# Kernel optimization log

Measured on AMD Instinct MI355X. Metric: run time of the kernel, lower is better.

The kernel has to match this reference:

```python
import jax, jax.numpy as jnp
import numpy as np

B_, C_, H_, W_ = 8, 128, 64, 64
OUT_ = 128
D_MODEL = C_ // 4        # 32, per-chunk channels fed to Mamba
D_STATE = 16
D_CONV = 4
D_INNER = 2 * D_MODEL    # expand=2 -> 64
DT_RANK = max(1, -(-D_MODEL // 16))  # ceil(32/16)=2
SE_RED = 2


def _ln(x, g, b):
    m = x.mean(-1, keepdims=True)
    v = jnp.var(x, axis=-1, keepdims=True)
    return (x - m) / jnp.sqrt(v + 1e-5) * g + b


def _mamba(u, in_W, conv_W, conv_b, xproj_W, dt_W, dt_b, A_log, D_p, out_W):
    # u: (B, L, d_model)
    Bsz, L, _ = u.shape
    xz = u @ in_W.T                                   # (B,L,2*d_inner)
    x, z = jnp.split(xz, 2, axis=-1)
    # causal depthwise conv1d along L
    xc = jnp.swapaxes(x, 1, 2)                        # (B,d_inner,L)
    xc = jax.lax.conv_general_dilated(
        xc, conv_W, (1,), [(D_CONV - 1, 0)],
        feature_group_count=D_INNER,
        dimension_numbers=('NCH', 'OIH', 'NCH'))
    x = jax.nn.silu(jnp.swapaxes(xc + conv_b[None, :, None], 1, 2))
    x_dbl = x @ xproj_W.T                             # (B,L,dt_rank+2*d_state)
    dt, Bm, Cm = jnp.split(x_dbl, [DT_RANK, DT_RANK + D_STATE], axis=-1)
    dt = jax.nn.softplus(dt @ dt_W.T + dt_b)          # (B,L,d_inner)
    A = -jnp.exp(A_log)                               # (d_inner,d_state)
    dA = jnp.exp(dt[..., None] * A)                   # (B,L,d_inner,d_state)
    dBu = dt[..., None] * Bm[:, :, None, :] * x[..., None]

    def step(h, inp):
        dA_t, dBu_t, C_t = inp
        h = dA_t * h + dBu_t                          # (B,d_inner,d_state)
        return h, jnp.einsum('bds,bs->bd', h, C_t)

    h0 = jnp.zeros((Bsz, D_INNER, D_STATE), dtype=x.dtype)
    _, ys = jax.lax.scan(step, h0, (jnp.swapaxes(dA, 0, 1), jnp.swapaxes(dBu, 0, 1), jnp.swapaxes(Cm, 0, 1)))
    y = jnp.swapaxes(ys, 0, 1) + x * D_p
    y = y * jax.nn.silu(z)
    return y @ out_W.T


def _branch(xi, skip_scale, se_W1, se_W2, mp):
    M1 = _mamba(xi, *mp)                              # (B,L,c)
    M2 = skip_scale * xi
    # SE: adaptive avg-pool over spatial == mean over tokens; cat over channels
    y = jnp.concatenate([M1, M2], axis=-1).mean(axis=1)   # (B,2c)
    y = jax.nn.sigmoid(jax.nn.relu(y @ se_W1.T) @ se_W2.T)
    g1, g2 = jnp.split(y, 2, axis=-1)
    return g1[:, None, :] * M1 + g2[:, None, :] * M2


def _pvm(x, norm_g, norm_b, proj_W, proj_b, skip_scale, se_W1, se_W2,
         in_W, conv_W, conv_b, xproj_W, dt_W, dt_b, A_log, D_p, out_W):
    B, C, H, W = x.shape
    L = H * W
    xf = jnp.swapaxes(x.reshape(B, C, L), 1, 2)       # (B,L,C)
    xn = _ln(xf, norm_g, norm_b)
    mp = (in_W, conv_W, conv_b, xproj_W, dt_W, dt_b, A_log, D_p, out_W)
    outs = [_branch(c, skip_scale, se_W1, se_W2, mp) for c in jnp.split(xn, 4, axis=2)]
    xm = jnp.concatenate(outs, axis=2)                # (B,L,C)
    xm = _ln(xm, norm_g, norm_b)
    xm = xm @ proj_W.T + proj_b                       # (B,L,out)
    return jnp.swapaxes(xm, 1, 2).reshape(B, proj_W.shape[0], H, W)


def setup_inputs():
    key = jax.random.key(0)
    ks = jax.random.split(key, 10)
    p = {}
    p['x'] = jax.random.normal(ks[0], (B_, C_, H_, W_), jnp.float32)
    p['norm_g'] = jnp.ones((C_,), jnp.float32)
    p['norm_b'] = jnp.zeros((C_,), jnp.float32)
    p['proj_W'] = jax.random.normal(ks[1], (OUT_, C_), jnp.float32) * 0.05
    p['proj_b'] = jnp.zeros((OUT_,), jnp.float32)
    p['skip_scale'] = jnp.ones((1,), jnp.float32)
    p['se_W1'] = jax.random.normal(ks[2], (SE_RED, 2 * D_MODEL), jnp.float32) * 0.1
    p['se_W2'] = jax.random.normal(ks[3], (2 * D_MODEL, SE_RED), jnp.float32) * 0.1
    p['in_W'] = jax.random.normal(ks[4], (2 * D_INNER, D_MODEL), jnp.float32) * 0.1
    p['conv_W'] = jax.random.normal(ks[5], (D_INNER, 1, D_CONV), jnp.float32) * 0.2
    p['conv_b'] = jnp.zeros((D_INNER,), jnp.float32)
    p['xproj_W'] = jax.random.normal(ks[6], (DT_RANK + 2 * D_STATE, D_INNER), jnp.float32) * 0.1
    p['dt_W'] = jax.random.normal(ks[7], (D_INNER, DT_RANK), jnp.float32) * 0.1
    p['dt_b'] = jnp.full((D_INNER,), -4.6, jnp.float32)  # softplus(-4.6) ~ 0.01 init dt
    p['A_log'] = jnp.log(jnp.broadcast_to(jnp.arange(1.0, D_STATE + 1.0, dtype=jnp.float32), (D_INNER, D_STATE)))
    p['D_p'] = jnp.ones((D_INNER,), jnp.float32)
    p['out_W'] = jax.random.normal(ks[8], (D_MODEL, D_INNER), jnp.float32) * 0.1
    return p


def reference(x, norm_g, norm_b, proj_W, proj_b, skip_scale, se_W1, se_W2,
              in_W, conv_W, conv_b, xproj_W, dt_W, dt_b, A_log, D_p, out_W):
    return _pvm(x, norm_g, norm_b, proj_W, proj_b, skip_scale, se_W1, se_W2,
                in_W, conv_W, conv_b, xproj_W, dt_W, dt_b, A_log, D_p, out_W)
```

## Files before the change

### kernel.cpp

```cpp
#include <hip/hip_runtime.h>
#include <math.h>

typedef _Float16 h16;

#define DEV static __device__ __forceinline__

constexpr int B_ = 8, C_ = 128, L_ = 4096, OUT_ = 128;
constexpr int NCH = 4, DM = 32, DS = 16, DI = 64;
constexpr int NI = 32;
constexpr int NSEG = 128;
constexpr int SL = L_ / NSEG;

DEV float sigmoidf_(float x) { return 1.f / (1.f + __expf(-x)); }
DEV float siluf_(float x) { return x * sigmoidf_(x); }
DEV float softplusf_(float x) { return (x > 20.f) ? x : __logf(1.f + __expf(x)); }

template <int CTRL>
DEV float dpp_add_(float x) {
  int v = __builtin_amdgcn_update_dpp(0, __float_as_int(x), CTRL, 0xf, 0xf, false);
  return x + __int_as_float(v);
}

typedef __attribute__((ext_vector_type(8))) _Float16 f16x8;
typedef __attribute__((ext_vector_type(4))) _Float16 f16x4;
typedef __attribute__((ext_vector_type(4))) float f32x4;

DEV void powladder_(float E, float* out) {
  float E2 = E * E;
  float E4 = E2 * E2;
  float E8 = E4 * E4;
  float E3 = E2 * E;
  out[0] = E;       out[1] = E2;      out[2] = E3;      out[3] = E4;
  out[4] = E4 * E;  out[5] = E4 * E2; out[6] = E4 * E3; out[7] = E8;
  out[8] = E8 * E;  out[9] = E8 * E2; out[10] = E8 * E3; out[11] = E8 * E4;
  out[12] = E8 * out[4]; out[13] = E8 * out[5]; out[14] = E8 * out[6];
  out[15] = E8 * E8;
}

DEV void powladder8_(float E, float* out) {
  float E2 = E * E, E3 = E2 * E, E4 = E2 * E2;
  out[0] = E; out[1] = E2; out[2] = E3; out[3] = E4;
  out[4] = E4 * E; out[5] = E4 * E2; out[6] = E4 * E3; out[7] = E4 * E4;
}

__global__ __launch_bounds__(256) void k1_ln(
    const float* __restrict__ x, const float* __restrict__ gn,
    const float* __restrict__ bn, const float* __restrict__ in_W,
    const float* __restrict__ xproj_W, const float* __restrict__ out_W,
    const float* __restrict__ proj_W, const float* __restrict__ A_log,
    h16* __restrict__ WH, float* __restrict__ AVT, h16* __restrict__ XNH,
    float* __restrict__ SUMXN) {
  int bid = blockIdx.x;
  int tid = threadIdx.x;
  if (bid >= B_ * 64) {
    int g = (bid - B_ * 64) * 256 + tid;
    if (g < 1024) AVT[g] = -__expf(A_log[g]);
    if (g < 4096) {
      WH[g] = (h16)in_W[g];
    } else if (g < 7168) {
      int j = g - 4096;
      int r = j >> 6;
      WH[g] = (r < 34) ? (h16)xproj_W[r * 64 + (j & 63)] : (h16)0.f;
    } else if (g < 9216) {
      WH[g] = (h16)out_W[g - 7168];
    } else if (g < 25600) {
      WH[g] = (h16)proj_W[g - 9216];
    }
    return;
  }
  int b = bid >> 6, tile = bid & 63;
  int t0 = tile * 64;
  __shared__ float xT[128][65];
  __shared__ float gnS[128], bnS[128];
  __shared__ float red[256];
  if (tid < 128) { gnS[tid] = gn[tid]; bnS[tid] = bn[tid]; }
  for (int k = tid; k < 8192; k += 256) {
    int c = k >> 6, tt = k & 63;
    xT[c][tt] = x[((size_t)(b * C_ + c)) * L_ + t0 + tt];
  }
  __syncthreads();
  {
    int tok = tid >> 2, q = tid & 3;
    float s = 0.f, qq = 0.f;
#pragma unroll
    for (int j = 0; j < 32; ++j) {
      float v = xT[q + 4 * j][tok];
      s += v; qq += v * v;
    }
    s = dpp_add_<0xB1>(s); qq = dpp_add_<0xB1>(qq);
    s = dpp_add_<0x4E>(s); qq = dpp_add_<0x4E>(qq);
    float m = s * (1.f / 128.f);
    float var = qq * (1.f / 128.f) - m * m;
    float rs = rsqrtf(var + 1e-5f);
#pragma unroll
    for (int j = 0; j < 32; ++j) {
      int c = q + 4 * j;
      float v = xT[c][tok];
      xT[c][tok] = (v - m) * rs * gnS[c] + bnS[c];
    }
  }
  __syncthreads();
  float acc = 0.f;
  int cfix = tid & 127;
  for (int k = tid; k < 8192; k += 256) {
    int tt = k >> 7, c = k & 127;
    acc += xT[c][tt];
  }
  for (int k = tid; k < 1024; k += 256) {
    int tt = k >> 4, c8 = (k & 15) * 8;
    f16x8 hv;
#pragma unroll
    for (int j = 0; j < 8; ++j) hv[j] = (_Float16)xT[c8 + j][tt];
    *(f16x8*)&XNH[((size_t)(b * L_ + t0 + tt)) * C_ + c8] = hv;
  }
  red[tid] = acc;
  __syncthreads();
  if (tid < 128) atomicAdd(&SUMXN[b * C_ + cfix], red[tid] + red[tid + 128]);
}

__global__ __launch_bounds__(256) void k2_prep(
    const h16* __restrict__ WH, const float* __restrict__ conv_W,
    const float* __restrict__ conv_b, const float* __restrict__ dt_W,
    const float* __restrict__ dt_b, const float* __restrict__ AVT,
    const h16* __restrict__ XNH, h16* __restrict__ SX2, h16* __restrict__ SDT2,
    h16* __restrict__ SB2, h16* __restrict__ SC2, h16* __restrict__ SZ2,
    h16* __restrict__ Pp, h16* __restrict__ Qp) {
  int bid = blockIdx.x;
  int i = bid >> 6, tile = bid & 63;
  int b = i >> 2, ch = i & 3;
  int t0 = tile * 64;
  int tid = threadIdx.x;
  int w = __builtin_amdgcn_readfirstlane(tid >> 6);
  int lane = tid & 63;

  __shared__ __attribute__((aligned(16))) union {
    _Float16 uH[80][40];
    float xdS[64][36];
    _Float16 zL[64][72];
  } U;
  __shared__ __attribute__((aligned(16))) _Float16 preH[68][68];
  __shared__ __attribute__((aligned(16))) _Float16 xH[64][72];
  __shared__ float convWS[64][4];
  __shared__ float dtWS[64][2];
  __shared__ float dtbS[64], cbS[64];

  convWS[tid >> 2][tid & 3] = conv_W[tid];
  if (tid < 128) dtWS[tid >> 1][tid & 1] = dt_W[tid];
  if (tid < 64) { dtbS[tid] = dt_b[tid]; cbS[tid] = conv_b[tid]; }
  const h16* xnh = XNH + (size_t)b * L_ * C_ + ch * DM;
  for (int k = tid; k < 320; k += 256) {
    int r = k >> 2, c8 = (k & 3) * 8;
    int tg = t0 - 3 + r;
    f16x8 v = {0, 0, 0, 0, 0, 0, 0, 0};
    if (r < 67 && tg >= 0) v = *(const f16x8*)&xnh[(size_t)tg * C_ + c8];
    *(f16x8*)&U.uH[r][c8] = v;
  }
  __syncthreads();

  int rsel = lane & 15, ksel = (lane >> 4) * 8;
  {
    int nt = w;
    f16x8 bf = *(const f16x8*)&WH[(size_t)(nt * 16 + rsel) * 32 + ksel];
    int row0q = (lane >> 4) << 2;
    int col = nt * 16 + rsel;
#pragma unroll
    for (int mt = 0; mt < 5; ++mt) {
      f16x8 af = *(const f16x8*)&U.uH[mt * 16 + rsel][ksel];
      f32x4 acc = {0.f, 0.f, 0.f, 0.f};
      acc = __builtin_amdgcn_mfma_f32_16x16x32_f16(af, bf, acc, 0, 0, 0);
      int row0 = mt * 16 + row0q;
#pragma unroll
      for (int r = 0; r < 4; ++r) {
        int row = row0 + r;
        if (row < 67) preH[row][col] = (_Float16)acc[r];
      }
    }
  }
  f32x4 zacc[4];
  {
    f16x8 bf = *(const f16x8*)&U.uH[3 + w * 16 + rsel][ksel];
#pragma unroll
    for (int mt = 0; mt < 4; ++mt) {
      f16x8 af = *(const f16x8*)&WH[(size_t)(64 + mt * 16 + rsel) * 32 + ksel];
      f32x4 acc = {0.f, 0.f, 0.f, 0.f};
      zacc[mt] = __builtin_amdgcn_mfma_f32_16x16x32_f16(af, bf, acc, 0, 0, 0);
    }
  }
  __syncthreads();

  h16* SXp = SX2 + ((size_t)i * L_ + t0) * DI;
  for (int k = tid; k < 4096; k += 256) {
    int r = k >> 6, d = k & 63;
    float v = cbS[d];
#pragma unroll
    for (int j = 0; j < 4; ++j) v = fmaf(convWS[d][j], (float)preH[r + j][d], v);
    v = siluf_(v);
    xH[r][d] = (_Float16)v;
    SXp[(size_t)r * DI + d] = (h16)v;
  }
  __syncthreads();

  {
    int mt = w;
    f16x8 a0 = *(const f16x8*)&xH[mt * 16 + rsel][ksel];
    f16x8 a1 = *(const f16x8*)&xH[mt * 16 + rsel][32 + ksel];
    int row0 = mt * 16 + ((lane >> 4) << 2);
#pragma unroll
    for (int nt = 0; nt < 3; ++nt) {
      const h16* wp = WH + 4096 + (size_t)(nt * 16 + rsel) * 64;
      f16x8 b0 = *(const f16x8*)&wp[ksel];
      f16x8 b1 = *(const f16x8*)&wp[32 + ksel];
      f32x4 acc = {0.f, 0.f, 0.f, 0.f};
      acc = __builtin_amdgcn_mfma_f32_16x16x32_f16(a0, b0, acc, 0, 0, 0);
      acc = __builtin_amdgcn_mfma_f32_16x16x32_f16(a1, b1, acc, 0, 0, 0);
      int col = nt * 16 + rsel;
      if (col < 34) {
#pragma unroll
        for (int r = 0; r < 4; ++r) U.xdS[row0 + r][col] = acc[r];
      }
    }
  }
  __syncthreads();

  h16* dtL = (h16*)&preH[0][0];
  h16* SDTp = SDT2 + ((size_t)i * L_ + t0) * DI;
  for (int k = tid; k < 4096; k += 256) {
    int d = k & 63, r = k >> 6;
    float raw = fmaf(U.xdS[r][0], dtWS[d][0], fmaf(U.xdS[r][1], dtWS[d][1], dtbS[d]));
    float dtv = softplusf_(raw);
    dtL[r * 68 + d] = (_Float16)dtv;
    SDTp[(size_t)r * DI + d] = (h16)dtv;
  }
  h16* SBp = SB2 + ((size_t)i * L_ + t0) * DS;
  h16* SCp = SC2 + ((size_t)i * L_ + t0) * DS;
  for (int k = tid; k < 1024; k += 256) {
    int s = k & 15, r = k >> 4;
    SBp[(size_t)r * DS + s] = (h16)U.xdS[r][2 + s];
    SCp[(size_t)r * DS + s] = (h16)U.xdS[r][18 + s];
  }
  __syncthreads();

  {
    int seg = w >> 1, shalf = w & 1;
    int s0 = shalf * 8;
    float Av[16];
    {
      const float* avp = AVT + lane * 16;
#pragma unroll
      for (int j = 0; j < 4; ++j) *(float4*)&Av[4 * j] = *(const float4*)(avp + 4 * j);
    }
    float A0 = Av[0];
    bool okf = true;
#pragma unroll
    for (int s = 0; s < 16; ++s)
      okf &= fabsf(Av[s] - (float)(s + 1) * A0) <= 1e-4f * fabsf(Av[s]);
    int fastp = __all(okf ? 1 : 0);
    float h[8];
#pragma unroll
    for (int j = 0; j < 8; ++j) h[j] = 0.f;
    float sdt = 0.f;
    int rowbase = seg * SL;
    for (int t = 0; t < SL; ++t) {
      int row = rowbase + t;
      float dt = (float)dtL[row * 68 + lane];
      float xv = (float)xH[row][lane];
      float dtx = dt * xv;
      float dA[8];
      if (fastp) {
        powladder8_(__expf(A0 * dt), dA);
        if (shalf) {
          float E8 = dA[7];
#pragma unroll
          for (int j = 0; j < 8; ++j) dA[j] *= E8;
        }
      } else {
#pragma unroll
        for (int j = 0; j < 8; ++j) dA[j] = __expf(Av[s0 + j] * dt);
      }
      const float* brow = &U.xdS[row][2 + s0];
#pragma unroll
      for (int j = 0; j < 8; ++j) h[j] = fmaf(dA[j], h[j], dtx * brow[j]);
      sdt += dt;
    }
    float P[8];
    if (fastp) {
      powladder8_(__expf(A0 * sdt), P);
      if (shalf) {
        float E8 = P[7];
#pragma unroll
        for (int j = 0; j < 8; ++j) P[j] *= E8;
      }
    } else {
#pragma unroll
      for (int j = 0; j < 8; ++j) P[j] = __expf(Av[s0 + j] * sdt);
    }
    int segg = tile * 2 + seg;
    size_t base = (((size_t)i * NSEG + segg) * DI + lane) * DS + s0;
    f16x8 ph, qh;
#pragma unroll
    for (int j = 0; j < 8; ++j) { ph[j] = (_Float16)P[j]; qh[j] = (_Float16)h[j]; }
    *(f16x8*)(Pp + base) = ph;
    *(f16x8*)(Qp + base) = qh;
  }
  __syncthreads();

  {
    int tok = w * 16 + rsel;
    int zq = (lane >> 4) << 2;
#pragma unroll
    for (int mt = 0; mt < 4; ++mt) {
      f16x4 pk;
#pragma unroll
      for (int r = 0; r < 4; ++r) pk[r] = (_Float16)siluf_(zacc[mt][r]);
      *(f16x4*)&U.zL[tok][mt * 16 + zq] = pk;
    }
  }
  __syncthreads();
  h16* SZp = SZ2 + ((size_t)i * L_ + t0) * DI;
  for (int k = tid; k < 512; k += 256) {
    int r = k >> 3, dblk = (k & 7) * 8;
    f16x8 v = *(const f16x8*)&U.zL[r][dblk];
    *(f16x8*)&SZp[(size_t)r * DI + dblk] = v;
  }
}

__global__ __launch_bounds__(64) void k3b_comb(h16* __restrict__ Pp,
                                               const h16* __restrict__ Qp) {
  int g = blockIdx.x * 64 + threadIdx.x;
  int ds = g & 1023;
  int i = g >> 10;
  size_t base = (size_t)i * NSEG * DI * DS + ds;
  constexpr int SST = DI * DS;
  float H = 0.f;
  for (int sb = 0; sb < NSEG; sb += 16) {
    float Pv[16], Qv[16];
#pragma unroll
    for (int j = 0; j < 16; ++j) {
      size_t a = base + (size_t)(sb + j) * SST;
      Pv[j] = (float)Pp[a];
      Qv[j] = (float)Qp[a];
    }
#pragma unroll
    for (int j = 0; j < 16; ++j) {
      size_t a = base + (size_t)(sb + j) * SST;
      Pp[a] = (h16)H;
      H = fmaf(Pv[j], H, Qv[j]);
    }
  }
}

__global__ __launch_bounds__(256) void k3c_scan(
    const float* __restrict__ AVT, const h16* __restrict__ SDT2,
    const h16* __restrict__ SX2, const h16* __restrict__ SB2,
    const h16* __restrict__ SC2, const h16* __restrict__ SZ2,
    const float* __restrict__ D_p, const h16* __restrict__ H0p,
    h16* __restrict__ YS2, float* __restrict__ SUMYF) {
  int bid = blockIdx.x;
  int i = bid >> 5, sg = bid & 31;
  int tid = threadIdx.x;
  int w = tid >> 6, lane = tid & 63;
  int seg = sg * 4 + w;
  int t0 = seg * SL;
  __shared__ float rowS[4][SL][36];
  {
    int tk = lane & 31, hf = lane >> 5;
    const h16* p = (hf ? SC2 : SB2) + ((size_t)i * L_ + t0 + tk) * DS;
    float4 r0 = *(const float4*)p;
    float4 r1 = *(const float4*)(p + 8);
    const h16* hp0 = (const h16*)&r0;
    const h16* hp1 = (const h16*)&r1;
#pragma unroll
    for (int s = 0; s < 8; ++s) {
      rowS[w][tk][hf * 16 + s] = (float)hp0[s];
      rowS[w][tk][hf * 16 + 8 + s] = (float)hp1[s];
    }
  }
  __syncthreads();
  float Av[16];
  {
    const float* avp = AVT + lane * 16;
#pragma unroll
    for (int j = 0; j < 4; ++j) *(float4*)&Av[4 * j] = *(const float4*)(avp + 4 * j);
  }
  float A0 = Av[0];
  bool okf = true;
#pragma unroll
  for (int s = 0; s < 16; ++s) okf &= fabsf(Av[s] - (float)(s + 1) * A0) <= 1e-4f * fabsf(Av[s]);
  int fastp = __all(okf ? 1 : 0);
  float Dp = D_p[lane];
  float h[16];
  {
    const h16* hp = H0p + (((size_t)i * NSEG + seg) * DI + lane) * DS;
    f16x8 h0a = *(const f16x8*)hp;
    f16x8 h0b = *(const f16x8*)(hp + 8);
#pragma unroll
    for (int j = 0; j < 8; ++j) { h[j] = (float)h0a[j]; h[8 + j] = (float)h0b[j]; }
  }
  const h16* pdt = SDT2 + ((size_t)i * L_ + t0) * DI + lane;
  const h16* pxx = SX2 + ((size_t)i * L_ + t0) * DI + lane;
  const h16* pzz = SZ2 + ((size_t)i * L_ + t0) * DI + lane;
  h16* pys = YS2 + ((size_t)i * L_ + t0) * DI + lane;
  float dtc = (float)pdt[0], xvc = (float)pxx[0], zvc = (float)pzz[0];
  float sum = 0.f;
  for (int t = 0; t < SL; ++t) {
    float dt = dtc, xv = xvc, zv = zvc;
    if (t < SL - 1) {
      dtc = (float)pdt[(t + 1) * DI];
      xvc = (float)pxx[(t + 1) * DI];
      zvc = (float)pzz[(t + 1) * DI];
    }
    const float* row = &rowS[w][t][0];
    float Bv[16], Cv[16];
#pragma unroll
    for (int j = 0; j < 4; ++j) {
      *(float4*)&Bv[4 * j] = *(const float4*)(row + 4 * j);
      *(float4*)&Cv[4 * j] = *(const float4*)(row + 16 + 4 * j);
    }
    float dtx = dt * xv;
    float dA[16];
    if (fastp) {
      powladder_(__expf(A0 * dt), dA);
    } else {
#pragma unroll
      for (int s = 0; s < 16; ++s) dA[s] = __expf(Av[s] * dt);
    }
    float y0 = 0.f, y1 = 0.f, y2 = 0.f, y3 = 0.f;
#pragma unroll
    for (int s = 0; s < 16; s += 4) {
      h[s] = fmaf(dA[s], h[s], dtx * Bv[s]);       y0 = fmaf(h[s], Cv[s], y0);
      h[s + 1] = fmaf(dA[s + 1], h[s + 1], dtx * Bv[s + 1]); y1 = fmaf(h[s + 1], Cv[s + 1], y1);
      h[s + 2] = fmaf(dA[s + 2], h[s + 2], dtx * Bv[s + 2]); y2 = fmaf(h[s + 2], Cv[s + 2], y2);
      h[s + 3] = fmaf(dA[s + 3], h[s + 3], dtx * Bv[s + 3]); y3 = fmaf(h[s + 3], Cv[s + 3], y3);
    }
    float y = (y0 + y1) + (y2 + y3);
    float yf = fmaf(xv, Dp, y) * zv;
    pys[(size_t)t * DI] = (h16)yf;
    sum += yf;
  }
  atomicAdd(&SUMYF[i * DI + lane], sum);
}

__global__ __launch_bounds__(256) void k56_comb_proj(
    const float* __restrict__ out_W, const float* __restrict__ skip_p,
    const float* __restrict__ se_W1, const float* __restrict__ se_W2,
    const float* __restrict__ SUMYF, const float* __restrict__ SUMXN,
    const h16* __restrict__ YS2, const float* __restrict__ gn,
    const float* __restrict__ bn, const h16* __restrict__ WH,
    const float* __restrict__ proj_b, const h16* __restrict__ XNH,
    float* __restrict__ out) {
  int bid = blockIdx.x;
  int b = bid >> 6, tile = bid & 63;
  int t0 = tile * 64;
  int tid = threadIdx.x;
  int w = __builtin_amdgcn_readfirstlane(tid >> 6);
  int lane = tid & 63;
  __shared__ __attribute__((aligned(16))) union {
    float xmS[64][132];
    _Float16 projH[64][136];
  } U;
  __shared__ __attribute__((aligned(16))) union {
    struct {
      _Float16 yH[64][72];
      _Float16 owH[32][72];
    } pre;
    _Float16 xmH[64][136];
  } V;
  __shared__ float gAll[4][64];
  __shared__ float gnS[128], bnS[128];
  float* catS = (float*)&V.pre.yH[0][0];
  float* seL = catS + 256;

  if (tid < 128) { gnS[tid] = gn[tid]; bnS[tid] = bn[tid]; }
  for (int k = tid; k < 256; k += 256) {
    int r = k >> 3, c8 = (k & 7) * 8;
    *(f16x8*)&V.pre.owH[r][c8] = *(const f16x8*)&WH[7168 + r * 64 + c8];
  }
  const h16* xmh = XNH + (size_t)b * L_ * C_;
  for (int k = tid; k < 1024; k += 256) {
    int tt = k >> 4, c8 = (k & 15) * 8;
    f16x8 hv = *(const f16x8*)&xmh[(size_t)(t0 + tt) * C_ + c8];
#pragma unroll
    for (int j = 0; j < 8; ++j) U.xmS[tt][c8 + j] = (float)hv[j];
  }
  {
    int ch = tid >> 6, j = tid & 63;
    float invL = 1.f / (float)L_;
    if (j < 32) {
      const float* sy = SUMYF + (b * 4 + ch) * DI;
      const float* ow = out_W + j * 64;
      float acc = 0.f;
#pragma unroll
      for (int dd = 0; dd < 64; ++dd) acc = fmaf(sy[dd], ow[dd], acc);
      catS[ch * 64 + j] = acc * invL;
    } else {
      catS[ch * 64 + j] = skip_p[0] * SUMXN[b * C_ + ch * DM + (j - 32)] * invL;
    }
  }
  __syncthreads();
  if (tid < 8) {
    int ch = tid >> 1, r = tid & 1;
    float acc = 0.f;
#pragma unroll
    for (int k = 0; k < 64; ++k) acc = fmaf(catS[ch * 64 + k], se_W1[r * 64 + k], acc);
    seL[tid] = fmaxf(acc, 0.f);
  }
  __syncthreads();
  {
    int ch = tid >> 6, j = tid & 63;
    gAll[ch][j] = sigmoidf_(fmaf(seL[ch * 2], se_W2[j * 2], seL[ch * 2 + 1] * se_W2[j * 2 + 1]));
  }
  __syncthreads();

  int rsel = lane & 15, ksel = (lane >> 4) * 8;
  float skip = skip_p[0];
  for (int ch = 0; ch < 4; ++ch) {
    const h16* py = YS2 + ((size_t)(b * 4 + ch) * L_ + t0) * DI;
    for (int k = tid; k < 512; k += 256) {
      int tt = k >> 3, dblk = (k & 7) * 8;
      *(f16x8*)&V.pre.yH[tt][dblk] = *(const f16x8*)&py[(size_t)tt * DI + dblk];
    }
    __syncthreads();
    f16x8 a0 = *(const f16x8*)&V.pre.yH[w * 16 + rsel][ksel];
    f16x8 a1 = *(const f16x8*)&V.pre.yH[w * 16 + rsel][32 + ksel];
    int row0 = w * 16 + ((lane >> 4) << 2);
#pragma unroll
    for (int nt = 0; nt < 2; ++nt) {
      f16x8 b0 = *(const f16x8*)&V.pre.owH[nt * 16 + rsel][ksel];
      f16x8 b1 = *(const f16x8*)&V.pre.owH[nt * 16 + rsel][32 + ksel];
      f32x4 acc = {0.f, 0.f, 0.f, 0.f};
      acc = __builtin_amdgcn_mfma_f32_16x16x32_f16(a0, b0, acc, 0, 0, 0);
      acc = __builtin_amdgcn_mfma_f32_16x16x32_f16(a1, b1, acc, 0, 0, 0);
      int o = nt * 16 + rsel;
      float g1 = gAll[ch][o], g2s = gAll[ch][32 + o] * skip;
      int cc = ch * 32 + o;
#pragma unroll
      for (int r = 0; r < 4; ++r) {
        int tok = row0 + r;
        U.xmS[tok][cc] = g1 * acc[r] + g2s * U.xmS[tok][cc];
      }
    }
    __syncthreads();
  }

  {
    int tok = tid >> 2, q = tid & 3;
    float s = 0.f, qq = 0.f;
#pragma unroll
    for (int j = 0; j < 32; ++j) {
      float v = U.xmS[tok][4 * j + q];
      s += v; qq += v * v;
    }
    s = dpp_add_<0xB1>(s); qq = dpp_add_<0xB1>(qq);
    s = dpp_add_<0x4E>(s); qq = dpp_add_<0x4E>(qq);
    float m = s * (1.f / 128.f);
    float var = qq * (1.f / 128.f) - m * m;
    float rs = rsqrtf(var + 1e-5f);
#pragma unroll
    for (int j = 0; j < 32; ++j) {
      int c = 4 * j + q;
      float v = U.xmS[tok][c];
      U.xmS[tok][c] = (v - m) * rs * gnS[c] + bnS[c];
    }
  }
  __syncthreads();
  for (int k = tid; k < 1024; k += 256) {
    int tt = k >> 4, cblk = (k & 15) * 8;
    float4 v0 = *(const float4*)&U.xmS[tt][cblk];
    float4 v1 = *(const float4*)&U.xmS[tt][cblk + 4];
    f16x8 hv;
    hv[0] = (_Float16)v0.x; hv[1] = (_Float16)v0.y;
    hv[2] = (_Float16)v0.z; hv[3] = (_Float16)v0.w;
    hv[4] = (_Float16)v1.x; hv[5] = (_Float16)v1.y;
    hv[6] = (_Float16)v1.z; hv[7] = (_Float16)v1.w;
    *(f16x8*)&V.xmH[tt][cblk] = hv;
  }
  __syncthreads();
  f16x8 af[4];
#pragma unroll
  for (int kc = 0; kc < 4; ++kc)
    af[kc] = *(const f16x8*)&V.xmH[w * 16 + rsel][kc * 32 + ksel];
  int row0 = w * 16 + ((lane >> 4) << 2);
#pragma unroll
  for (int half = 0; half < 2; ++half) {
    for (int k = tid; k < 1024; k += 256) {
      int o = k >> 4, cblk = (k & 15) * 8;
      *(f16x8*)&U.projH[o][cblk] =
          *(const f16x8*)&WH[9216 + (half * 64 + o) * 128 + cblk];
    }
    __syncthreads();
#pragma unroll
    for (int nt = 0; nt < 4; ++nt) {
      int ol = nt * 16 + rsel;
      int o = half * 64 + ol;
      float pb = proj_b[o];
      f32x4 acc = {pb, pb, pb, pb};
#pragma unroll
      for (int kc = 0; kc < 4; ++kc) {
        f16x8 bf = *(const f16x8*)&U.projH[ol][kc * 32 + ksel];
        acc = __builtin_amdgcn_mfma_f32_16x16x32_f16(af[kc], bf, acc, 0, 0, 0);
      }
      *(float4*)&out[((size_t)(b * OUT_ + o)) * L_ + t0 + row0] =
          make_float4(acc[0], acc[1], acc[2], acc[3]);
    }
    __syncthreads();
  }
}

extern "C" void kernel_launch(void* const* d_in, const int* in_sizes, int n_in,
                              void* d_out, int out_size, void* d_ws, size_t ws_size,
                              hipStream_t stream) {
  const float* x = (const float*)d_in[0];
  const float* norm_g = (const float*)d_in[1];
  const float* norm_b = (const float*)d_in[2];
  const float* proj_W = (const float*)d_in[3];
  const float* proj_b = (const float*)d_in[4];
  const float* skip = (const float*)d_in[5];
  const float* se_W1 = (const float*)d_in[6];
  const float* se_W2 = (const float*)d_in[7];
  const float* in_W = (const float*)d_in[8];
  const float* conv_W = (const float*)d_in[9];
  const float* conv_b = (const float*)d_in[10];
  const float* xproj_W = (const float*)d_in[11];
  const float* dt_W = (const float*)d_in[12];
  const float* dt_b = (const float*)d_in[13];
  const float* A_log = (const float*)d_in[14];
  const float* D_p = (const float*)d_in[15];
  const float* out_W = (const float*)d_in[16];
  float* out = (float*)d_out;

  float* SUMYF = (float*)d_ws;
  float* SUMXN = SUMYF + NI * DI;
  h16* Pp = (h16*)(SUMXN + B_ * C_);
  h16* Qp = Pp + (size_t)NI * DI * NSEG * DS;
  h16* YS2 = Qp + (size_t)NI * DI * NSEG * DS;
  h16* SX2 = YS2 + (size_t)NI * L_ * DI;
  h16* SDT2 = SX2 + (size_t)NI * L_ * DI;
  h16* SB2 = SDT2 + (size_t)NI * L_ * DI;
  h16* SC2 = SB2 + (size_t)NI * L_ * DS;
  h16* SZ2 = SC2 + (size_t)NI * L_ * DS;
  h16* XNH = SZ2 + (size_t)NI * L_ * DI;
  h16* WH = XNH + (size_t)B_ * L_ * C_;
  float* AVT = (float*)(WH + 25600);

  hipMemsetAsync(SUMYF, 0, (size_t)(NI * DI + B_ * C_) * sizeof(float), stream);
  k1_ln<<<B_ * 64 + 104, 256, 0, stream>>>(x, norm_g, norm_b, in_W, xproj_W,
                                           out_W, proj_W, A_log, WH, AVT, XNH,
                                           SUMXN);
  k2_prep<<<NI * 64, 256, 0, stream>>>(WH, conv_W, conv_b, dt_W, dt_b, AVT,
                                       XNH, SX2, SDT2, SB2, SC2, SZ2, Pp, Qp);
  k3b_comb<<<512, 64, 0, stream>>>(Pp, Qp);
  k3c_scan<<<NI * 32, 256, 0, stream>>>(AVT, SDT2, SX2, SB2, SC2, SZ2, D_p,
                                        Pp, YS2, SUMYF);
  k56_comb_proj<<<B_ * 64, 256, 0, stream>>>(out_W, skip, se_W1, se_W2, SUMYF,
                                             SUMXN, YS2, norm_g, norm_b, WH,
                                             proj_b, XNH, out);
}
```

Baseline: 204.8 us.

## Fuse Mamba out_proj MFMA into scan kernel and store projected output

The scan kernel now stages its per-token y values in shared memory and applies the out_W projection (64->32) with MFMA before writing to global, storing YM in a channel-major layout. The combine/projection kernel then reads the already-projected 32-wide result instead of the 64-wide y and no longer runs the per-chunk MFMA loop with its syncs. This halves the intermediate y traffic between kernels and removes work from the final kernel. In exchange the scan kernel gets more shared memory and a strided scalar store pattern, and the xmS padding changes to 133, which may affect bank conflicts.

```diff
diff --git a/kernel.cpp b/kernel.cpp
--- a/kernel.cpp
+++ b/kernel.cpp
@@ -354,7 +354,8 @@
     const h16* __restrict__ SX2, const h16* __restrict__ SB2,
     const h16* __restrict__ SC2, const h16* __restrict__ SZ2,
     const float* __restrict__ D_p, const h16* __restrict__ H0p,
-    h16* __restrict__ YS2, float* __restrict__ SUMYF) {
+    const h16* __restrict__ WH, h16* __restrict__ YM,
+    float* __restrict__ SUMYF) {
   int bid = blockIdx.x;
   int i = bid >> 5, sg = bid & 31;
   int tid = threadIdx.x;
@@ -362,6 +363,7 @@
   int seg = sg * 4 + w;
   int t0 = seg * SL;
   __shared__ float rowS[4][SL][36];
+  __shared__ __attribute__((aligned(16))) _Float16 yfL[4][SL][66];
   {
     int tk = lane & 31, hf = lane >> 5;
     const h16* p = (hf ? SC2 : SB2) + ((size_t)i * L_ + t0 + tk) * DS;
@@ -399,7 +401,6 @@
   const h16* pdt = SDT2 + ((size_t)i * L_ + t0) * DI + lane;
   const h16* pxx = SX2 + ((size_t)i * L_ + t0) * DI + lane;
   const h16* pzz = SZ2 + ((size_t)i * L_ + t0) * DI + lane;
-  h16* pys = YS2 + ((size_t)i * L_ + t0) * DI + lane;
   float dtc = (float)pdt[0], xvc = (float)pxx[0], zvc = (float)pzz[0];
   float sum = 0.f;
   for (int t = 0; t < SL; ++t) {
@@ -434,17 +435,43 @@
     }
     float y = (y0 + y1) + (y2 + y3);
     float yf = fmaf(xv, Dp, y) * zv;
-    pys[(size_t)t * DI] = (h16)yf;
+    yfL[w][t][lane] = (_Float16)yf;
     sum += yf;
   }
   atomicAdd(&SUMYF[i * DI + lane], sum);
+  __syncthreads();
+
+  {
+    int rsel = lane & 15, ksel = (lane >> 4) * 8;
+    int rq = (lane >> 4) << 2;
+#pragma unroll
+    for (int ot = 0; ot < 2; ++ot) {
+      const h16* wo = WH + 7168 + (size_t)(ot * 16 + rsel) * 64;
+      f16x8 af0 = *(const f16x8*)&wo[ksel];
+      f16x8 af1 = *(const f16x8*)&wo[32 + ksel];
+#pragma unroll
+      for (int tt = 0; tt < 2; ++tt) {
+        f16x8 b0 = *(const f16x8*)&yfL[w][tt * 16 + rsel][ksel];
+        f16x8 b1 = *(const f16x8*)&yfL[w][tt * 16 + rsel][32 + ksel];
+        f32x4 acc = {0.f, 0.f, 0.f, 0.f};
+        acc = __builtin_amdgcn_mfma_f32_16x16x32_f16(af0, b0, acc, 0, 0, 0);
+        acc = __builtin_amdgcn_mfma_f32_16x16x32_f16(af1, b1, acc, 0, 0, 0);
+        int tloc = tt * 16 + rsel;
+#pragma unroll
+        for (int r = 0; r < 4; ++r) {
+          int o = ot * 16 + rq + r;
+          YM[((size_t)i * 32 + o) * L_ + t0 + tloc] = (h16)acc[r];
+        }
+      }
+    }
+  }
 }
 
 __global__ __launch_bounds__(256) void k56_comb_proj(
     const float* __restrict__ out_W, const float* __restrict__ skip_p,
     const float* __restrict__ se_W1, const float* __restrict__ se_W2,
     const float* __restrict__ SUMYF, const float* __restrict__ SUMXN,
-    const h16* __restrict__ YS2, const float* __restrict__ gn,
+    const h16* __restrict__ YM, const float* __restrict__ gn,
     const float* __restrict__ bn, const h16* __restrict__ WH,
     const float* __restrict__ proj_b, const h16* __restrict__ XNH,
     float* __restrict__ out) {
@@ -455,26 +482,16 @@
   int w = __builtin_amdgcn_readfirstlane(tid >> 6);
   int lane = tid & 63;
   __shared__ __attribute__((aligned(16))) union {
-    float xmS[64][132];
+    float xmS[64][133];
     _Float16 projH[64][136];
   } U;
-  __shared__ __attribute__((aligned(16))) union {
-    struct {
-      _Float16 yH[64][72];
-      _Float16 owH[32][72];
-    } pre;
-    _Float16 xmH[64][136];
-  } V;
+  __shared__ __attribute__((aligned(16))) _Float16 xmH[64][136];
   __shared__ float gAll[4][64];
   __shared__ float gnS[128], bnS[128];
-  float* catS = (float*)&V.pre.yH[0][0];
+  float* catS = (float*)&xmH[0][0];
   float* seL = catS + 256;
 
   if (tid < 128) { gnS[tid] = gn[tid]; bnS[tid] = bn[tid]; }
-  for (int k = tid; k < 256; k += 256) {
-    int r = k >> 3, c8 = (k & 7) * 8;
-    *(f16x8*)&V.pre.owH[r][c8] = *(const f16x8*)&WH[7168 + r * 64 + c8];
-  }
   const h16* xmh = XNH + (size_t)b * L_ * C_;
   for (int k = tid; k < 1024; k += 256) {
     int tt = k >> 4, c8 = (k & 15) * 8;
@@ -511,36 +528,20 @@
   }
   __syncthreads();
 
-  int rsel = lane & 15, ksel = (lane >> 4) * 8;
   float skip = skip_p[0];
-  for (int ch = 0; ch < 4; ++ch) {
-    const h16* py = YS2 + ((size_t)(b * 4 + ch) * L_ + t0) * DI;
-    for (int k = tid; k < 512; k += 256) {
-      int tt = k >> 3, dblk = (k & 7) * 8;
-      *(f16x8*)&V.pre.yH[tt][dblk] = *(const f16x8*)&py[(size_t)tt * DI + dblk];
-    }
-    __syncthreads();
-    f16x8 a0 = *(const f16x8*)&V.pre.yH[w * 16 + rsel][ksel];
-    f16x8 a1 = *(const f16x8*)&V.pre.yH[w * 16 + rsel][32 + ksel];
-    int row0 = w * 16 + ((lane >> 4) << 2);
-#pragma unroll
-    for (int nt = 0; nt < 2; ++nt) {
-      f16x8 b0 = *(const f16x8*)&V.pre.owH[nt * 16 + rsel][ksel];
-      f16x8 b1 = *(const f16x8*)&V.pre.owH[nt * 16 + rsel][32 + ksel];
-      f32x4 acc = {0.f, 0.f, 0.f, 0.f};
-      acc = __builtin_amdgcn_mfma_f32_16x16x32_f16(a0, b0, acc, 0, 0, 0);
-      acc = __builtin_amdgcn_mfma_f32_16x16x32_f16(a1, b1, acc, 0, 0, 0);
-      int o = nt * 16 + rsel;
-      float g1 = gAll[ch][o], g2s = gAll[ch][32 + o] * skip;
-      int cc = ch * 32 + o;
-#pragma unroll
-      for (int r = 0; r < 4; ++r) {
-        int tok = row0 + r;
-        U.xmS[tok][cc] = g1 * acc[r] + g2s * U.xmS[tok][cc];
-      }
-    }
-    __syncthreads();
-  }
+  for (int k = tid; k < 1024; k += 256) {
+    int ch = k >> 8;
+    int o = (k >> 3) & 31;
+    int t8 = (k & 7) * 8;
+    const h16* pym = YM + (((size_t)(b * 4 + ch) * 32 + o)) * L_ + t0 + t8;
+    f16x8 ym8 = *(const f16x8*)pym;
+    float g1 = gAll[ch][o], g2s = gAll[ch][32 + o] * skip;
+    int cc = ch * 32 + o;
+#pragma unroll
+    for (int j = 0; j < 8; ++j)
+      U.xmS[t8 + j][cc] = fmaf(g1, (float)ym8[j], g2s * U.xmS[t8 + j][cc]);
+  }
+  __syncthreads();
 
   {
     int tok = tid >> 2, q = tid & 3;
@@ -572,13 +573,14 @@
     hv[2] = (_Float16)v0.z; hv[3] = (_Float16)v0.w;
     hv[4] = (_Float16)v1.x; hv[5] = (_Float16)v1.y;
     hv[6] = (_Float16)v1.z; hv[7] = (_Float16)v1.w;
-    *(f16x8*)&V.xmH[tt][cblk] = hv;
-  }
-  __syncthreads();
+    *(f16x8*)&xmH[tt][cblk] = hv;
+  }
+  __syncthreads();
+  int rsel = lane & 15, ksel = (lane >> 4) * 8;
   f16x8 af[4];
 #pragma unroll
   for (int kc = 0; kc < 4; ++kc)
-    af[kc] = *(const f16x8*)&V.xmH[w * 16 + rsel][kc * 32 + ksel];
+    af[kc] = *(const f16x8*)&xmH[w * 16 + rsel][kc * 32 + ksel];
   int row0 = w * 16 + ((lane >> 4) << 2);
 #pragma unroll
   for (int half = 0; half < 2; ++half) {
@@ -632,8 +634,8 @@
   float* SUMXN = SUMYF + NI * DI;
   h16* Pp = (h16*)(SUMXN + B_ * C_);
   h16* Qp = Pp + (size_t)NI * DI * NSEG * DS;
-  h16* YS2 = Qp + (size_t)NI * DI * NSEG * DS;
-  h16* SX2 = YS2 + (size_t)NI * L_ * DI;
+  h16* YM = Qp + (size_t)NI * DI * NSEG * DS;
+  h16* SX2 = YM + (size_t)NI * 32 * L_;
   h16* SDT2 = SX2 + (size_t)NI * L_ * DI;
   h16* SB2 = SDT2 + (size_t)NI * L_ * DI;
   h16* SC2 = SB2 + (size_t)NI * L_ * DS;
@@ -650,8 +652,8 @@
                                        XNH, SX2, SDT2, SB2, SC2, SZ2, Pp, Qp);
   k3b_comb<<<512, 64, 0, stream>>>(Pp, Qp);
   k3c_scan<<<NI * 32, 256, 0, stream>>>(AVT, SDT2, SX2, SB2, SC2, SZ2, D_p,
-                                        Pp, YS2, SUMYF);
+                                        Pp, WH, YM, SUMYF);
   k56_comb_proj<<<B_ * 64, 256, 0, stream>>>(out_W, skip, se_W1, se_W2, SUMYF,
-                                             SUMXN, YS2, norm_g, norm_b, WH,
+                                             SUMXN, YM, norm_g, norm_b, WH,
                                              proj_b, XNH, out);
 }
```

Result: no change. 205.7 us (+0.5%).
